# Kernel tuning notes

Measured on AMD Instinct MI355X. Metric: run time of the kernel, lower is better.

Reference implementation:

```python
import jax, jax.numpy as jnp
import numpy as np

N = 131072      # number of nodes / samples
IN_DIM = 128    # input_dim
H = 128         # hidden_dim
OUT_DIM = 10    # output_dim


def setup_inputs() -> dict:
    key = jax.random.key(0)
    ks = jax.random.split(key, 20)
    s = 0.05
    def rn(k, shape):
        return jax.random.normal(k, shape, jnp.float32) * s
    return {
        "x": jax.random.normal(ks[0], (N, IN_DIM), jnp.float32),
        # GRU layer 1 (seq_len=1, h0=0 => weight_hh contributes nothing; only b_hh matters)
        "w_ih_f1": rn(ks[1], (3 * H, IN_DIM)), "b_ih_f1": rn(ks[2], (3 * H,)), "b_hh_f1": rn(ks[3], (3 * H,)),
        "w_ih_b1": rn(ks[4], (3 * H, IN_DIM)), "b_ih_b1": rn(ks[5], (3 * H,)), "b_hh_b1": rn(ks[6], (3 * H,)),
        # GRU layer 2 (input 2H)
        "w_ih_f2": rn(ks[7], (3 * H, 2 * H)), "b_ih_f2": rn(ks[8], (3 * H,)), "b_hh_f2": rn(ks[9], (3 * H,)),
        "w_ih_b2": rn(ks[10], (3 * H, 2 * H)), "b_ih_b2": rn(ks[11], (3 * H,)), "b_hh_b2": rn(ks[12], (3 * H,)),
        # GCNConv layers
        "w_g1": rn(ks[13], (2 * H, 128)), "b_g1": rn(ks[14], (128,)),
        "w_g2": rn(ks[15], (128, 64)), "b_g2": rn(ks[16], (64,)),
        # final fc
        "w_fc": rn(ks[17], (64, OUT_DIM)), "b_fc": rn(ks[18], (OUT_DIM,)),
    }


def _gru_cell_zero(x, w_ih, b_ih, b_hh):
    # PyTorch GRU cell with h_prev = 0: h' = (1 - z) * n_gate
    gi = x @ w_ih.T + b_ih                    # [n, 3H]
    ir, iz, inn = jnp.split(gi, 3, axis=-1)
    hr, hz, hn = jnp.split(b_hh, 3)
    r = jax.nn.sigmoid(ir + hr)
    z = jax.nn.sigmoid(iz + hz)
    ng = jnp.tanh(inn + r * hn)
    return (1.0 - z) * ng


def _gcn(x, w, b, sources, targets, n):
    # PyG GCNConv: D^{-1/2}(A+I)D^{-1/2} X W + b, self-loops already in edge lists
    xw = x @ w                                 # [n, out]
    deg = jax.ops.segment_sum(jnp.ones(sources.shape[0], x.dtype), targets, num_segments=n)
    dinv = jax.lax.rsqrt(deg)
    norm = dinv[sources] * dinv[targets]       # [E]
    msg = norm[:, None] * xw[sources]          # gather
    return jax.ops.segment_sum(msg, targets, num_segments=n) + b  # scatter-add


def reference(x, w_ih_f1, b_ih_f1, b_hh_f1, w_ih_b1, b_ih_b1, b_hh_b1,
              w_ih_f2, b_ih_f2, b_hh_f2, w_ih_b2, b_ih_b2, b_hh_b2,
              w_g1, b_g1, w_g2, b_g2, w_fc, b_fc):
    n = x.shape[0]
    # seq_len = 1 => bidirectional GRU output is [fwd_cell(x); bwd_cell(x)]
    h1 = jnp.concatenate([_gru_cell_zero(x, w_ih_f1, b_ih_f1, b_hh_f1),
                          _gru_cell_zero(x, w_ih_b1, b_ih_b1, b_hh_b1)], axis=-1)
    h2 = jnp.concatenate([_gru_cell_zero(h1, w_ih_f2, b_ih_f2, b_hh_f2),
                          _gru_cell_zero(h1, w_ih_b2, b_ih_b2, b_hh_b2)], axis=-1)
    # chain graph, both directions, plus self loops (GCNConv adds them)
    src = jnp.arange(n - 1)
    dst = jnp.arange(1, n)
    ar = jnp.arange(n)
    sources = jnp.concatenate([src, dst, ar])
    targets = jnp.concatenate([dst, src, ar])
    g1 = _gcn(h2, w_g1, b_g1, sources, targets, n)   # dropout is identity in eval
    g2 = _gcn(g1, w_g2, b_g2, sources, targets, n)
    return g2 @ w_fc + b_fc
```

## Files before the change

### kernel.cpp

```cpp
#include <hip/hip_runtime.h>
#include <stdint.h>

#define N_NODES 131072
#define HDIM 128

typedef __bf16 bf16x8 __attribute__((ext_vector_type(8)));
typedef float f32x4 __attribute__((ext_vector_type(4)));
typedef unsigned short us8 __attribute__((ext_vector_type(8)));
typedef unsigned short ushort_t;

__device__ __forceinline__ float bf2f(ushort_t u) {
    union { float f; uint32_t i; } v; v.i = ((uint32_t)u) << 16; return v.f;
}
__device__ __forceinline__ ushort_t f2bf(float f) {
    union { float f; uint32_t i; } v; v.f = f;
    uint32_t i = v.i;
    return (ushort_t)((i + 0x7FFFu + ((i >> 16) & 1u)) >> 16);
}

__device__ __forceinline__ void gll16(const ushort_t* g, ushort_t* l) {
    __builtin_amdgcn_global_load_lds(
        (const __attribute__((address_space(1))) uint32_t*)g,
        (__attribute__((address_space(3))) uint32_t*)l, 16, 0, 0);
}

__device__ __forceinline__ bf16x8 ldsw(const ushort_t* base, int R, int g) {
    return *(const bf16x8*)&base[R * 64 + (((g - R) & 7) << 3)];
}

__device__ __forceinline__ float fsig(float x) {
    return __builtin_amdgcn_rcpf(1.0f + __expf(-x));
}
__device__ __forceinline__ float ftanh(float y) {
    float yc = fminf(fmaxf(y, -15.0f), 15.0f);
    float e = __expf(2.0f * yc);
    return (e - 1.0f) * __builtin_amdgcn_rcpf(e + 1.0f);
}

template<int NC>
__device__ __forceinline__ void swz(int b, int& m, int& c) {
    int mhi = b / (8 * NC);
    int rem = b - mhi * (8 * NC);
    c = rem >> 3;
    m = mhi * 8 + (rem & 7);
}

__global__ __launch_bounds__(256) void prep_weights(
    const float* __restrict__ w_f1, const float* __restrict__ w_b1,
    const float* __restrict__ w_f2, const float* __restrict__ w_b2,
    const float* __restrict__ w_g1, const float* __restrict__ w_g2,
    ushort_t* __restrict__ PWF1, ushort_t* __restrict__ PWB1,
    ushort_t* __restrict__ PWF2, ushort_t* __restrict__ PWB2,
    ushort_t* __restrict__ WT1,  ushort_t* __restrict__ WT2)
{
    int idx = blockIdx.x * 256 + threadIdx.x;
    if (idx < 49152) {
        PWF1[idx] = f2bf(w_f1[idx]);
    } else if (idx < 98304) {
        int j = idx - 49152;  PWB1[j] = f2bf(w_b1[j]);
    } else if (idx < 196608) {
        int j = idx - 98304;  PWF2[j] = f2bf(w_f2[j]);
    } else if (idx < 294912) {
        int j = idx - 196608; PWB2[j] = f2bf(w_b2[j]);
    } else if (idx < 327680) {
        int j = idx - 294912; int k = j >> 7, o = j & 127;
        WT1[o * 256 + k] = f2bf(w_g1[j]);
    } else if (idx < 335872) {
        int j = idx - 327680; int k = j >> 6, o = j & 63;
        WT2[o * 128 + k] = f2bf(w_g2[j]);
    }
}

__global__ __launch_bounds__(256) void xconv(
    const float* __restrict__ x, ushort_t* __restrict__ xb)
{
    int idx = blockIdx.x * 256 + threadIdx.x;
    const float* s = x + (size_t)idx * 8;
    float4 f0 = ((const float4*)s)[0];
    float4 f1 = ((const float4*)s)[1];
    us8 t;
    t[0] = f2bf(f0.x); t[1] = f2bf(f0.y); t[2] = f2bf(f0.z); t[3] = f2bf(f0.w);
    t[4] = f2bf(f1.x); t[5] = f2bf(f1.y); t[6] = f2bf(f1.z); t[7] = f2bf(f1.w);
    *(us8*)&xb[(size_t)idx * 8] = t;
}

template<int K>
__global__ __launch_bounds__(256, 5) void gru_gemm2(
    const ushort_t* __restrict__ A,
    const ushort_t* __restrict__ Wf,
    const ushort_t* __restrict__ Wb,
    const float* __restrict__ bi_f, const float* __restrict__ bh_f,
    const float* __restrict__ bi_b, const float* __restrict__ bh_b,
    ushort_t* __restrict__ Hout)
{
    __shared__ ushort_t As[128 * 64];
    __shared__ ushort_t Bs[96 * 64];
    const int tid = threadIdx.x;
    int mt, comb;
    swz<8>(blockIdx.x, mt, comb);
    const int m0 = mt * 128;
    const int dir = comb >> 2;
    const int j0 = (comb & 3) * 32;
    const ushort_t* W = dir ? Wb : Wf;
    const float* b_ih = dir ? bi_b : bi_f;
    const float* b_hh = dir ? bh_b : bh_f;
    const int coloff = dir << 7;

    const int wv = tid >> 6, lane = tid & 63;
    const int lr = lane & 15, lq = lane >> 4;
    const int tr = tid >> 3, tc = tid & 7;
    const int sc = ((tr + tc) & 7) << 3;

    f32x4 acc[3][2][2];
    #pragma unroll
    for (int g = 0; g < 3; ++g)
        #pragma unroll
        for (int rt = 0; rt < 2; ++rt)
            #pragma unroll
            for (int ct = 0; ct < 2; ++ct)
                #pragma unroll
                for (int e = 0; e < 4; ++e) acc[g][rt][ct][e] = 0.0f;

    for (int t = 0; t < K / 64; ++t) {
        const int k0 = t * 64;
        const ushort_t* ga = A + (size_t)(m0 + tr) * K + k0 + sc;
        #pragma unroll
        for (int i = 0; i < 4; ++i)
            gll16(ga + (size_t)i * 32 * K, &As[(i * 256 + tid) * 8]);
        #pragma unroll
        for (int i = 0; i < 3; ++i) {
            int wr = (i << 7) + j0 + tr;
            gll16(W + (size_t)wr * K + k0 + sc, &Bs[(i * 256 + tid) * 8]);
        }
        __syncthreads();
        #pragma unroll
        for (int kk = 0; kk < 64; kk += 32) {
            const int g8 = (kk >> 3) + lq;
            bf16x8 a0 = ldsw(As, wv * 32 + lr, g8);
            bf16x8 a1 = ldsw(As, wv * 32 + 16 + lr, g8);
            #pragma unroll
            for (int g = 0; g < 3; ++g) {
                #pragma unroll
                for (int ct = 0; ct < 2; ++ct) {
                    bf16x8 b = ldsw(Bs, g * 32 + ct * 16 + lr, g8);
                    acc[g][0][ct] = __builtin_amdgcn_mfma_f32_16x16x32_bf16(a0, b, acc[g][0][ct], 0, 0, 0);
                    acc[g][1][ct] = __builtin_amdgcn_mfma_f32_16x16x32_bf16(a1, b, acc[g][1][ct], 0, 0, 0);
                }
            }
        }
        __syncthreads();
    }

    #pragma unroll
    for (int ct = 0; ct < 2; ++ct) {
        const int j = j0 + ct * 16 + lr;
        const float br  = b_ih[j] + b_hh[j];
        const float bz  = b_ih[HDIM + j] + b_hh[HDIM + j];
        const float bn  = b_ih[2 * HDIM + j];
        const float bhn = b_hh[2 * HDIM + j];
        #pragma unroll
        for (int rt = 0; rt < 2; ++rt) {
            #pragma unroll
            for (int r = 0; r < 4; ++r) {
                const int row = m0 + wv * 32 + rt * 16 + lq * 4 + r;
                float rg = fsig(acc[0][rt][ct][r] + br);
                float zg = fsig(acc[1][rt][ct][r] + bz);
                float ng = ftanh(acc[2][rt][ct][r] + bn + rg * bhn);
                Hout[(size_t)row * 256 + coloff + j] = f2bf((1.0f - zg) * ng);
            }
        }
    }
}

template<int K, int NC>
__global__ __launch_bounds__(256, 5) void gemm_bt2(
    const ushort_t* __restrict__ A,
    const ushort_t* __restrict__ Wt,
    ushort_t* __restrict__ Out,
    int Nld)
{
    __shared__ ushort_t As[128 * 64];
    __shared__ ushort_t Bs[64 * 64];
    const int tid = threadIdx.x;
    int mt, nc;
    swz<NC>(blockIdx.x, mt, nc);
    const int m0 = mt * 128;
    const int n0 = nc * 64;
    const int wv = tid >> 6, lane = tid & 63;
    const int lr = lane & 15, lq = lane >> 4;
    const int tr = tid >> 3, tc = tid & 7;
    const int sc = ((tr + tc) & 7) << 3;

    f32x4 acc[2][4];
    #pragma unroll
    for (int rt = 0; rt < 2; ++rt)
        #pragma unroll
        for (int ct = 0; ct < 4; ++ct)
            #pragma unroll
            for (int e = 0; e < 4; ++e) acc[rt][ct][e] = 0.0f;

    for (int t = 0; t < K / 64; ++t) {
        const int k0 = t * 64;
        const ushort_t* ga = A + (size_t)(m0 + tr) * K + k0 + sc;
        #pragma unroll
        for (int i = 0; i < 4; ++i)
            gll16(ga + (size_t)i * 32 * K, &As[(i * 256 + tid) * 8]);
        const ushort_t* gb = Wt + (size_t)(n0 + tr) * K + k0 + sc;
        #pragma unroll
        for (int i = 0; i < 2; ++i)
            gll16(gb + (size_t)i * 32 * K, &Bs[(i * 256 + tid) * 8]);
        __syncthreads();
        #pragma unroll
        for (int kk = 0; kk < 64; kk += 32) {
            const int g8 = (kk >> 3) + lq;
            bf16x8 a0 = ldsw(As, wv * 32 + lr, g8);
            bf16x8 a1 = ldsw(As, wv * 32 + 16 + lr, g8);
            #pragma unroll
            for (int ct = 0; ct < 4; ++ct) {
                bf16x8 b = ldsw(Bs, ct * 16 + lr, g8);
                acc[0][ct] = __builtin_amdgcn_mfma_f32_16x16x32_bf16(a0, b, acc[0][ct], 0, 0, 0);
                acc[1][ct] = __builtin_amdgcn_mfma_f32_16x16x32_bf16(a1, b, acc[1][ct], 0, 0, 0);
            }
        }
        __syncthreads();
    }

    #pragma unroll
    for (int ct = 0; ct < 4; ++ct) {
        const int col = n0 + ct * 16 + lr;
        #pragma unroll
        for (int rt = 0; rt < 2; ++rt) {
            #pragma unroll
            for (int r = 0; r < 4; ++r) {
                const int row = m0 + wv * 32 + rt * 16 + lq * 4 + r;
                Out[(size_t)row * Nld + col] = f2bf(acc[rt][ct][r]);
            }
        }
    }
}

__global__ __launch_bounds__(256) void stencil8(
    const ushort_t* __restrict__ xw, const float* __restrict__ bias,
    ushort_t* __restrict__ g)
{
    const float S2 = 0.70710678118654752f, S3 = 0.57735026918962576f;
    int idx = blockIdx.x * 256 + threadIdx.x;
    int i = idx >> 4, c8 = (idx & 15) << 3;
    float di = (i == 0 || i == N_NODES - 1) ? S2 : S3;
    bool hm = i > 0, hp = i < N_NODES - 1;
    float dm = hm ? ((i - 1 == 0) ? S2 : S3) : 0.0f;
    float dp = hp ? ((i + 1 == N_NODES - 1) ? S2 : S3) : 0.0f;
    us8 v0 = *(const us8*)(xw + (size_t)i * 128 + c8);
    us8 vm = *(const us8*)(xw + (size_t)(hm ? i - 1 : i) * 128 + c8);
    us8 vp = *(const us8*)(xw + (size_t)(hp ? i + 1 : i) * 128 + c8);
    us8 o;
    #pragma unroll
    for (int e = 0; e < 8; ++e) {
        float s = di * bf2f(v0[e]) + dm * bf2f(vm[e]) + dp * bf2f(vp[e]);
        o[e] = f2bf(di * s + bias[c8 + e]);
    }
    *(us8*)&g[(size_t)i * 128 + c8] = o;
}

__global__ __launch_bounds__(256) void final_fc(
    const ushort_t* __restrict__ xw2,
    const float* __restrict__ b_g2,
    const float* __restrict__ w_fc,
    const float* __restrict__ b_fc,
    float* __restrict__ out)
{
    __shared__ float wfc_s[640];
    __shared__ float bg2_s[64];
    __shared__ float bfc_s[10];
    const int tid = threadIdx.x;
    for (int t = tid; t < 640; t += 256) wfc_s[t] = w_fc[t];
    if (tid < 64) bg2_s[tid] = b_g2[tid];
    if (tid < 10) bfc_s[tid] = b_fc[tid];
    __syncthreads();

    const float S2 = 0.70710678118654752f, S3 = 0.57735026918962576f;
    const int i = blockIdx.x * 256 + tid;
    float di = (i == 0 || i == N_NODES - 1) ? S2 : S3;
    bool hm = i > 0, hp = i < N_NODES - 1;
    float dm = hm ? ((i - 1 == 0) ? S2 : S3) : 0.0f;
    float dp = hp ? ((i + 1 == N_NODES - 1) ? S2 : S3) : 0.0f;
    const ushort_t* r0 = xw2 + (size_t)i * 64;
    const ushort_t* rm = xw2 + (size_t)(hm ? i - 1 : i) * 64;
    const ushort_t* rp = xw2 + (size_t)(hp ? i + 1 : i) * 64;

    float o[10];
    #pragma unroll
    for (int k = 0; k < 10; ++k) o[k] = bfc_s[k];
    #pragma unroll
    for (int c8 = 0; c8 < 8; ++c8) {
        us8 v0 = *(const us8*)&r0[c8 * 8];
        us8 vm = *(const us8*)&rm[c8 * 8];
        us8 vp = *(const us8*)&rp[c8 * 8];
        #pragma unroll
        for (int e = 0; e < 8; ++e) {
            int c = c8 * 8 + e;
            float s = di * bf2f(v0[e]) + dm * bf2f(vm[e]) + dp * bf2f(vp[e]);
            float g2 = di * s + bg2_s[c];
            #pragma unroll
            for (int k = 0; k < 10; ++k) o[k] += g2 * wfc_s[c * 10 + k];
        }
    }
    #pragma unroll
    for (int k = 0; k < 10; ++k) out[(size_t)i * 10 + k] = o[k];
}

extern "C" void kernel_launch(void* const* d_in, const int* in_sizes, int n_in,
                              void* d_out, int out_size, void* d_ws, size_t ws_size,
                              hipStream_t stream) {
    const float* x     = (const float*)d_in[0];
    const float* w_f1  = (const float*)d_in[1];
    const float* bi_f1 = (const float*)d_in[2];
    const float* bh_f1 = (const float*)d_in[3];
    const float* w_b1  = (const float*)d_in[4];
    const float* bi_b1 = (const float*)d_in[5];
    const float* bh_b1 = (const float*)d_in[6];
    const float* w_f2  = (const float*)d_in[7];
    const float* bi_f2 = (const float*)d_in[8];
    const float* bh_f2 = (const float*)d_in[9];
    const float* w_b2  = (const float*)d_in[10];
    const float* bi_b2 = (const float*)d_in[11];
    const float* bh_b2 = (const float*)d_in[12];
    const float* w_g1  = (const float*)d_in[13];
    const float* b_g1  = (const float*)d_in[14];
    const float* w_g2  = (const float*)d_in[15];
    const float* b_g2  = (const float*)d_in[16];
    const float* w_fc  = (const float*)d_in[17];
    const float* b_fc  = (const float*)d_in[18];

    char* ws = (char*)d_ws;
    ushort_t* h1   = (ushort_t*)(ws);
    ushort_t* xb   = (ushort_t*)(ws + 67108864);
    ushort_t* h2   = (ushort_t*)(ws + 67108864);
    ushort_t* xw1  = (ushort_t*)(ws);
    ushort_t* g1   = (ushort_t*)(ws + 33554432);
    ushort_t* xw2  = (ushort_t*)(ws + 67108864);
    ushort_t* PWF1 = (ushort_t*)(ws + 134217728);
    ushort_t* PWB1 = PWF1 + 49152;
    ushort_t* PWF2 = PWB1 + 49152;
    ushort_t* PWB2 = PWF2 + 98304;
    ushort_t* WT1  = PWB2 + 98304;
    ushort_t* WT2  = WT1 + 32768;

    prep_weights<<<1312, 256, 0, stream>>>(w_f1, w_b1, w_f2, w_b2, w_g1, w_g2,
                                           PWF1, PWB1, PWF2, PWB2, WT1, WT2);
    xconv<<<N_NODES * 16 / 256, 256, 0, stream>>>(x, xb);

    gru_gemm2<128><<<N_NODES / 128 * 8, 256, 0, stream>>>(
        xb, PWF1, PWB1, bi_f1, bh_f1, bi_b1, bh_b1, h1);
    gru_gemm2<256><<<N_NODES / 128 * 8, 256, 0, stream>>>(
        h1, PWF2, PWB2, bi_f2, bh_f2, bi_b2, bh_b2, h2);

    gemm_bt2<256, 2><<<N_NODES / 128 * 2, 256, 0, stream>>>(h2, WT1, xw1, 128);
    stencil8<<<N_NODES * 16 / 256, 256, 0, stream>>>(xw1, b_g1, g1);
    gemm_bt2<128, 1><<<N_NODES / 128, 256, 0, stream>>>(g1, WT2, xw2, 64);
    final_fc<<<N_NODES / 256, 256, 0, stream>>>(xw2, b_g2, w_fc, b_fc, (float*)d_out);
}
```

Before: 303.7 us.

## Fold GCN and FC weights into one 256x10 matrix, apply stencils after

Since the GCN layers have no nonlinearity, the change precomputes M = W_g1·W_g2·W_fc and the bias contributions in a small prep kernel. It then runs one thin GEMM from h2 to 10 columns and applies the normalized chain stencil twice on 10-wide float data. This removes the wide 256→128 and 128→64 GEMMs and the 128-wide stencil traffic. The trade-off is rounding the combined matrix to bf16, plus a single-block prep kernel that serializes some work.

```diff
diff --git a/kernel.cpp b/kernel.cpp
--- a/kernel.cpp
+++ b/kernel.cpp
@@ -48,10 +48,8 @@
 __global__ __launch_bounds__(256) void prep_weights(
     const float* __restrict__ w_f1, const float* __restrict__ w_b1,
     const float* __restrict__ w_f2, const float* __restrict__ w_b2,
-    const float* __restrict__ w_g1, const float* __restrict__ w_g2,
     ushort_t* __restrict__ PWF1, ushort_t* __restrict__ PWB1,
-    ushort_t* __restrict__ PWF2, ushort_t* __restrict__ PWB2,
-    ushort_t* __restrict__ WT1,  ushort_t* __restrict__ WT2)
+    ushort_t* __restrict__ PWF2, ushort_t* __restrict__ PWB2)
 {
     int idx = blockIdx.x * 256 + threadIdx.x;
     if (idx < 49152) {
@@ -62,12 +60,43 @@
         int j = idx - 98304;  PWF2[j] = f2bf(w_f2[j]);
     } else if (idx < 294912) {
         int j = idx - 196608; PWB2[j] = f2bf(w_b2[j]);
-    } else if (idx < 327680) {
-        int j = idx - 294912; int k = j >> 7, o = j & 127;
-        WT1[o * 256 + k] = f2bf(w_g1[j]);
-    } else if (idx < 335872) {
-        int j = idx - 327680; int k = j >> 6, o = j & 63;
-        WT2[o * 128 + k] = f2bf(w_g2[j]);
+    }
+}
+
+__global__ __launch_bounds__(256) void prep_M(
+    const float* __restrict__ w_g1, const float* __restrict__ b_g1,
+    const float* __restrict__ w_g2, const float* __restrict__ b_g2,
+    const float* __restrict__ w_fc, const float* __restrict__ b_fc,
+    ushort_t* __restrict__ M16, float* __restrict__ cc)
+{
+    __shared__ float T1[128][10];
+    const int t = threadIdx.x;
+    if (t < 128) {
+        #pragma unroll
+        for (int j = 0; j < 10; ++j) {
+            float s = 0.0f;
+            for (int k3 = 0; k3 < 64; ++k3) s += w_g2[t * 64 + k3] * w_fc[k3 * 10 + j];
+            T1[t][j] = s;
+        }
+    }
+    __syncthreads();
+    float m[10];
+    #pragma unroll
+    for (int j = 0; j < 10; ++j) {
+        float s = 0.0f;
+        for (int k2 = 0; k2 < 128; ++k2) s += w_g1[t * 128 + k2] * T1[k2][j];
+        m[j] = s;
+    }
+    #pragma unroll
+    for (int j = 0; j < 16; ++j)
+        M16[j * 256 + t] = (j < 10) ? f2bf(m[j]) : (ushort_t)0;
+    if (t < 10) {
+        float s1 = 0.0f;
+        for (int k2 = 0; k2 < 128; ++k2) s1 += b_g1[k2] * T1[k2][t];
+        cc[t] = s1;
+        float s2 = 0.0f;
+        for (int k3 = 0; k3 < 64; ++k3) s2 += b_g2[k3] * w_fc[k3 * 10 + t];
+        cc[16 + t] = s2 + b_fc[t];
     }
 }
 
@@ -172,141 +201,77 @@
     }
 }
 
-template<int K, int NC>
-__global__ __launch_bounds__(256, 5) void gemm_bt2(
+__global__ __launch_bounds__(256, 5) void zgemm(
     const ushort_t* __restrict__ A,
-    const ushort_t* __restrict__ Wt,
-    ushort_t* __restrict__ Out,
-    int Nld)
+    const ushort_t* __restrict__ M16,
+    float* __restrict__ Zc)
 {
     __shared__ ushort_t As[128 * 64];
-    __shared__ ushort_t Bs[64 * 64];
     const int tid = threadIdx.x;
-    int mt, nc;
-    swz<NC>(blockIdx.x, mt, nc);
-    const int m0 = mt * 128;
-    const int n0 = nc * 64;
+    const int m0 = blockIdx.x * 128;
     const int wv = tid >> 6, lane = tid & 63;
     const int lr = lane & 15, lq = lane >> 4;
     const int tr = tid >> 3, tc = tid & 7;
     const int sc = ((tr + tc) & 7) << 3;
 
-    f32x4 acc[2][4];
-    #pragma unroll
-    for (int rt = 0; rt < 2; ++rt)
-        #pragma unroll
-        for (int ct = 0; ct < 4; ++ct)
-            #pragma unroll
-            for (int e = 0; e < 4; ++e) acc[rt][ct][e] = 0.0f;
-
-    for (int t = 0; t < K / 64; ++t) {
+    bf16x8 bfrag[8];
+    #pragma unroll
+    for (int s = 0; s < 8; ++s)
+        bfrag[s] = *(const bf16x8*)&M16[lr * 256 + s * 32 + lq * 8];
+
+    f32x4 acc[2];
+    #pragma unroll
+    for (int e = 0; e < 4; ++e) { acc[0][e] = 0.0f; acc[1][e] = 0.0f; }
+
+    for (int t = 0; t < 4; ++t) {
         const int k0 = t * 64;
-        const ushort_t* ga = A + (size_t)(m0 + tr) * K + k0 + sc;
+        const ushort_t* ga = A + (size_t)(m0 + tr) * 256 + k0 + sc;
         #pragma unroll
         for (int i = 0; i < 4; ++i)
-            gll16(ga + (size_t)i * 32 * K, &As[(i * 256 + tid) * 8]);
-        const ushort_t* gb = Wt + (size_t)(n0 + tr) * K + k0 + sc;
-        #pragma unroll
-        for (int i = 0; i < 2; ++i)
-            gll16(gb + (size_t)i * 32 * K, &Bs[(i * 256 + tid) * 8]);
+            gll16(ga + (size_t)i * 32 * 256, &As[(i * 256 + tid) * 8]);
         __syncthreads();
         #pragma unroll
         for (int kk = 0; kk < 64; kk += 32) {
             const int g8 = (kk >> 3) + lq;
             bf16x8 a0 = ldsw(As, wv * 32 + lr, g8);
             bf16x8 a1 = ldsw(As, wv * 32 + 16 + lr, g8);
-            #pragma unroll
-            for (int ct = 0; ct < 4; ++ct) {
-                bf16x8 b = ldsw(Bs, ct * 16 + lr, g8);
-                acc[0][ct] = __builtin_amdgcn_mfma_f32_16x16x32_bf16(a0, b, acc[0][ct], 0, 0, 0);
-                acc[1][ct] = __builtin_amdgcn_mfma_f32_16x16x32_bf16(a1, b, acc[1][ct], 0, 0, 0);
-            }
+            bf16x8 b = bfrag[t * 2 + (kk >> 5)];
+            acc[0] = __builtin_amdgcn_mfma_f32_16x16x32_bf16(a0, b, acc[0], 0, 0, 0);
+            acc[1] = __builtin_amdgcn_mfma_f32_16x16x32_bf16(a1, b, acc[1], 0, 0, 0);
         }
         __syncthreads();
     }
 
-    #pragma unroll
-    for (int ct = 0; ct < 4; ++ct) {
-        const int col = n0 + ct * 16 + lr;
-        #pragma unroll
-        for (int rt = 0; rt < 2; ++rt) {
+    if (lr < 10) {
+        #pragma unroll
+        for (int rt = 0; rt < 2; ++rt)
             #pragma unroll
             for (int r = 0; r < 4; ++r) {
-                const int row = m0 + wv * 32 + rt * 16 + lq * 4 + r;
-                Out[(size_t)row * Nld + col] = f2bf(acc[rt][ct][r]);
+                int row = m0 + wv * 32 + rt * 16 + lq * 4 + r;
+                Zc[(size_t)row * 10 + lr] = acc[rt][r];
             }
-        }
-    }
-}
-
-__global__ __launch_bounds__(256) void stencil8(
-    const ushort_t* __restrict__ xw, const float* __restrict__ bias,
-    ushort_t* __restrict__ g)
-{
-    const float S2 = 0.70710678118654752f, S3 = 0.57735026918962576f;
+    }
+}
+
+__device__ __forceinline__ float dcoef(int i) {
+    return (i == 0 || i == N_NODES - 1) ? 0.70710678118654752f : 0.57735026918962576f;
+}
+template<int FIN>
+__global__ __launch_bounds__(256) void stencil10(
+    const float* __restrict__ in, float* __restrict__ out,
+    const float* __restrict__ cc)
+{
     int idx = blockIdx.x * 256 + threadIdx.x;
-    int i = idx >> 4, c8 = (idx & 15) << 3;
-    float di = (i == 0 || i == N_NODES - 1) ? S2 : S3;
-    bool hm = i > 0, hp = i < N_NODES - 1;
-    float dm = hm ? ((i - 1 == 0) ? S2 : S3) : 0.0f;
-    float dp = hp ? ((i + 1 == N_NODES - 1) ? S2 : S3) : 0.0f;
-    us8 v0 = *(const us8*)(xw + (size_t)i * 128 + c8);
-    us8 vm = *(const us8*)(xw + (size_t)(hm ? i - 1 : i) * 128 + c8);
-    us8 vp = *(const us8*)(xw + (size_t)(hp ? i + 1 : i) * 128 + c8);
-    us8 o;
-    #pragma unroll
-    for (int e = 0; e < 8; ++e) {
-        float s = di * bf2f(v0[e]) + dm * bf2f(vm[e]) + dp * bf2f(vp[e]);
-        o[e] = f2bf(di * s + bias[c8 + e]);
-    }
-    *(us8*)&g[(size_t)i * 128 + c8] = o;
-}
-
-__global__ __launch_bounds__(256) void final_fc(
-    const ushort_t* __restrict__ xw2,
-    const float* __restrict__ b_g2,
-    const float* __restrict__ w_fc,
-    const float* __restrict__ b_fc,
-    float* __restrict__ out)
-{
-    __shared__ float wfc_s[640];
-    __shared__ float bg2_s[64];
-    __shared__ float bfc_s[10];
-    const int tid = threadIdx.x;
-    for (int t = tid; t < 640; t += 256) wfc_s[t] = w_fc[t];
-    if (tid < 64) bg2_s[tid] = b_g2[tid];
-    if (tid < 10) bfc_s[tid] = b_fc[tid];
-    __syncthreads();
-
-    const float S2 = 0.70710678118654752f, S3 = 0.57735026918962576f;
-    const int i = blockIdx.x * 256 + tid;
-    float di = (i == 0 || i == N_NODES - 1) ? S2 : S3;
-    bool hm = i > 0, hp = i < N_NODES - 1;
-    float dm = hm ? ((i - 1 == 0) ? S2 : S3) : 0.0f;
-    float dp = hp ? ((i + 1 == N_NODES - 1) ? S2 : S3) : 0.0f;
-    const ushort_t* r0 = xw2 + (size_t)i * 64;
-    const ushort_t* rm = xw2 + (size_t)(hm ? i - 1 : i) * 64;
-    const ushort_t* rp = xw2 + (size_t)(hp ? i + 1 : i) * 64;
-
-    float o[10];
-    #pragma unroll
-    for (int k = 0; k < 10; ++k) o[k] = bfc_s[k];
-    #pragma unroll
-    for (int c8 = 0; c8 < 8; ++c8) {
-        us8 v0 = *(const us8*)&r0[c8 * 8];
-        us8 vm = *(const us8*)&rm[c8 * 8];
-        us8 vp = *(const us8*)&rp[c8 * 8];
-        #pragma unroll
-        for (int e = 0; e < 8; ++e) {
-            int c = c8 * 8 + e;
-            float s = di * bf2f(v0[e]) + dm * bf2f(vm[e]) + dp * bf2f(vp[e]);
-            float g2 = di * s + bg2_s[c];
-            #pragma unroll
-            for (int k = 0; k < 10; ++k) o[k] += g2 * wfc_s[c * 10 + k];
-        }
-    }
-    #pragma unroll
-    for (int k = 0; k < 10; ++k) out[(size_t)i * 10 + k] = o[k];
+    int i = idx >> 4, c = idx & 15;
+    if (c >= 10) return;
+    float di = dcoef(i);
+    float s = di * in[(size_t)i * 10 + c];
+    float dsum = di;
+    if (i > 0)           { float dm = dcoef(i - 1); s += dm * in[(size_t)(i - 1) * 10 + c]; dsum += dm; }
+    if (i < N_NODES - 1) { float dp = dcoef(i + 1); s += dp * in[(size_t)(i + 1) * 10 + c]; dsum += dp; }
+    float r = di * s;
+    if (FIN) r += di * dsum * cc[c] + cc[16 + c];
+    out[(size_t)i * 10 + c] = r;
 }
 
 extern "C" void kernel_launch(void* const* d_in, const int* in_sizes, int n_in,
@@ -336,18 +301,18 @@
     ushort_t* h1   = (ushort_t*)(ws);
     ushort_t* xb   = (ushort_t*)(ws + 67108864);
     ushort_t* h2   = (ushort_t*)(ws + 67108864);
-    ushort_t* xw1  = (ushort_t*)(ws);
-    ushort_t* g1   = (ushort_t*)(ws + 33554432);
-    ushort_t* xw2  = (ushort_t*)(ws + 67108864);
+    float*    Zc   = (float*)(ws);
+    float*    u    = (float*)(ws + 8388608);
     ushort_t* PWF1 = (ushort_t*)(ws + 134217728);
     ushort_t* PWB1 = PWF1 + 49152;
     ushort_t* PWF2 = PWB1 + 49152;
     ushort_t* PWB2 = PWF2 + 98304;
-    ushort_t* WT1  = PWB2 + 98304;
-    ushort_t* WT2  = WT1 + 32768;
-
-    prep_weights<<<1312, 256, 0, stream>>>(w_f1, w_b1, w_f2, w_b2, w_g1, w_g2,
-                                           PWF1, PWB1, PWF2, PWB2, WT1, WT2);
+    ushort_t* M16  = PWB2 + 98304;
+    float*    cc   = (float*)(M16 + 4096);
+
+    prep_weights<<<1152, 256, 0, stream>>>(w_f1, w_b1, w_f2, w_b2,
+                                           PWF1, PWB1, PWF2, PWB2);
+    prep_M<<<1, 256, 0, stream>>>(w_g1, b_g1, w_g2, b_g2, w_fc, b_fc, M16, cc);
     xconv<<<N_NODES * 16 / 256, 256, 0, stream>>>(x, xb);
 
     gru_gemm2<128><<<N_NODES / 128 * 8, 256, 0, stream>>>(
@@ -355,8 +320,7 @@
     gru_gemm2<256><<<N_NODES / 128 * 8, 256, 0, stream>>>(
         h1, PWF2, PWB2, bi_f2, bh_f2, bi_b2, bh_b2, h2);
 
-    gemm_bt2<256, 2><<<N_NODES / 128 * 2, 256, 0, stream>>>(h2, WT1, xw1, 128);
-    stencil8<<<N_NODES * 16 / 256, 256, 0, stream>>>(xw1, b_g1, g1);
-    gemm_bt2<128, 1><<<N_NODES / 128, 256, 0, stream>>>(g1, WT2, xw2, 64);
-    final_fc<<<N_NODES / 256, 256, 0, stream>>>(xw2, b_g2, w_fc, b_fc, (float*)d_out);
-}
+    zgemm<<<N_NODES / 128, 256, 0, stream>>>(h2, M16, Zc);
+    stencil10<0><<<N_NODES * 16 / 256, 256, 0, stream>>>(Zc, u, cc);
+    stencil10<1><<<N_NODES * 16 / 256, 256, 0, stream>>>(u, (float*)d_out, cc);
+}
```

Result: slower. 336.1 us (+10.7%).
